# Performance work log

Measured on AMD Instinct MI355X. Metric: run time of the kernel, lower is better.

## Reference

```python
import jax, jax.numpy as jnp
import numpy as np

N = 50000       # nodes
E = 1_600_000   # edges (avg degree 32)
IN = 256        # in_dim
HID = 64        # hidden_dim
HEADS = 2
CLS = 10
NEG_SLOPE = 0.2  # PyG GATConv default leaky_relu slope


def gat_layer(x, edge_index, W, att_src, att_dst, bias, heads, concat):
    """PyG-style GATConv (eval mode, add_self_loops=True).
    x: [N, F_in]; W: [F_in, heads*C]; att_src/att_dst: [heads, C]; bias: [heads*C] or [C].
    """
    n = x.shape[0]
    loop = jnp.arange(n)
    src = jnp.concatenate([edge_index[0], loop])   # message sources j
    dst = jnp.concatenate([edge_index[1], loop])   # message targets i
    C = W.shape[1] // heads
    h = (x @ W).reshape(n, heads, C)               # [N, H, C]
    a_s = jnp.sum(h * att_src, axis=-1)            # [N, H]
    a_d = jnp.sum(h * att_dst, axis=-1)            # [N, H]
    e = jax.nn.leaky_relu(a_s[src] + a_d[dst], NEG_SLOPE)   # [E', H]
    # segment softmax over incoming edges of each destination node
    m = jax.lax.stop_gradient(jax.ops.segment_max(e, dst, num_segments=n))
    ex = jnp.exp(e - m[dst])
    denom = jax.ops.segment_sum(ex, dst, num_segments=n)
    alpha = ex / denom[dst]                         # [E', H]
    out = jax.ops.segment_sum(alpha[:, :, None] * h[src], dst, num_segments=n)  # [N, H, C]
    out = out.reshape(n, heads * C) if concat else out.mean(axis=1)
    return out + bias


def setup_inputs() -> dict:
    key = jax.random.key(0)
    ks = jax.random.split(key, 12)
    sd = lambda f: np.float32(1.0 / np.sqrt(f))
    x = jax.random.normal(ks[0], (N, IN), dtype=jnp.float32)
    edge_index = jax.random.randint(ks[1], (2, E), 0, N, dtype=jnp.int64)
    # layer 1: in_dim -> hidden, heads=2, concat
    W1 = jax.random.normal(ks[2], (IN, HEADS * HID), dtype=jnp.float32) * sd(IN)
    as1 = jax.random.normal(ks[3], (HEADS, HID), dtype=jnp.float32) * sd(HID)
    ad1 = jax.random.normal(ks[4], (HEADS, HID), dtype=jnp.float32) * sd(HID)
    b1 = jnp.zeros((HEADS * HID,), dtype=jnp.float32)
    # layer 2: hidden*heads -> hidden, heads=1, concat=False
    W2 = jax.random.normal(ks[5], (HEADS * HID, HID), dtype=jnp.float32) * sd(HEADS * HID)
    as2 = jax.random.normal(ks[6], (1, HID), dtype=jnp.float32) * sd(HID)
    ad2 = jax.random.normal(ks[7], (1, HID), dtype=jnp.float32) * sd(HID)
    b2 = jnp.zeros((HID,), dtype=jnp.float32)
    # linear head
    Wl = jax.random.normal(ks[8], (HID, CLS), dtype=jnp.float32) * sd(HID)
    bl = jnp.zeros((CLS,), dtype=jnp.float32)
    return {"x": x, "edge_index": edge_index,
            "W1": W1, "as1": as1, "ad1": ad1, "b1": b1,
            "W2": W2, "as2": as2, "ad2": ad2, "b2": b2,
            "Wl": Wl, "bl": bl}


def reference(x, edge_index, W1, as1, ad1, b1, W2, as2, ad2, b2, Wl, bl):
    h = jax.nn.elu(gat_layer(x, edge_index, W1, as1, ad1, b1, HEADS, True))
    h = jax.nn.elu(gat_layer(h, edge_index, W2, as2, ad2, b2, 1, False))
    return h @ Wl + bl  # [N, num_classes]
```

## Files before the change

### kernel.cpp

```cpp
#include <hip/hip_runtime.h>

#define NN 50000
#define NE 1600000
#define EP (NE + NN)
#define IN_DIM 256
#define HIDD 64
#define NCLS 10
#define NBKT 196
#define EPB 8192
#define NPB ((EP + EPB - 1) / EPB)
#define BCAP 12288

typedef unsigned short u16;
typedef short bf16x8 __attribute__((ext_vector_type(8)));
typedef float f32x4 __attribute__((ext_vector_type(4)));

__device__ __forceinline__ float b2f(u16 v) { return __uint_as_float(((unsigned)v) << 16); }
__device__ __forceinline__ u16 f2b(float f) {
    unsigned u = __float_as_uint(f);
    unsigned r = (u + 0x7FFFu + ((u >> 16) & 1u)) >> 16;
    return (u16)r;
}

__device__ __forceinline__ void load_edge(const int* __restrict__ ei, int m, int g,
                                          int& s, int& d) {
    if (g < NE) {
        if (m) { s = ei[2 * (size_t)g]; d = ei[2 * ((size_t)NE + g)]; }
        else   { s = ei[g];             d = ei[NE + g]; }
    } else {
        s = d = g - NE;
    }
    s = s < 0 ? 0 : (s >= NN ? NN - 1 : s);
    d = d < 0 ? 0 : (d >= NN ? NN - 1 : d);
}

__device__ __forceinline__ void wcvt_att_job(
    const float* __restrict__ W, const float* __restrict__ as,
    const float* __restrict__ ad, int K, int N, int H, u16* __restrict__ Wt,
    int idx) {
    if (idx >= K * (N + 16)) return;
    int n = idx / K, k = idx - n * K;
    if (n < N) { Wt[idx] = f2b(W[(size_t)k * N + n]); return; }
    int j = n - N;
    if (j >= 2 * H) { Wt[idx] = 0; return; }
    const float* att = (j & 1) ? ad : as;
    int h = j >> 1, C = N / H;
    float sum = 0.f;
    for (int c = 0; c < C; ++c)
        sum += W[(size_t)k * N + h * C + c] * att[h * C + c];
    Wt[idx] = f2b(sum);
}

__global__ __launch_bounds__(1024) void partition_k(
    const int* __restrict__ ei, int* __restrict__ gcursor,
    unsigned* __restrict__ bbuf,
    const float* __restrict__ W1, const float* __restrict__ as1,
    const float* __restrict__ ad1, u16* __restrict__ w1t,
    const float* __restrict__ W2, const float* __restrict__ as2,
    const float* __restrict__ ad2, u16* __restrict__ w2t,
    const float* __restrict__ Wl, u16* __restrict__ wlt) {
    __shared__ int hist[NBKT], base[NBKT], lbase[NBKT], lcur[NBKT];
    __shared__ int psc[256];
    __shared__ unsigned sst[EPB];
    __shared__ int smode;
    int t = threadIdx.x, b = blockIdx.x;
    if (b < 36) wcvt_att_job(W1, as1, ad1, 256, 128, 2, w1t, b * 1024 + t);
    else if (b < 46) wcvt_att_job(W2, as2, ad2, 128, 64, 1, w2t, (b - 36) * 1024 + t);
    else if (b == 46) {
        int n = t >> 6, k = t & 63;
        wlt[n * 64 + k] = (n < NCLS) ? f2b(Wl[k * NCLS + n]) : (u16)0;
    }
    if (t < 64) {
        int nz = 0;
#pragma unroll
        for (int k = 0; k < 4; ++k)
            if (ei[2 * (t * 4 + k) + 1] != 0) nz = 1;
        unsigned long long bal = __ballot(nz);
        if (t == 0) smode = (bal == 0ULL) ? 1 : 0;
    }
    for (int i = t; i < NBKT; i += 1024) hist[i] = 0;
    __syncthreads();
    int m = smode;
    int g0 = b * EPB;
    int gend = min(g0 + EPB, EP);
    for (int g = g0 + t; g < gend; g += 1024) {
        int s, d;
        load_edge(ei, m, g, s, d);
        atomicAdd(&hist[d >> 8], 1);
    }
    __syncthreads();
    int hv = 0;
    if (t < 256) { hv = (t < NBKT) ? hist[t] : 0; psc[t] = hv; }
    __syncthreads();
    for (int off = 1; off < 256; off <<= 1) {
        int x = (t < 256 && t >= off) ? psc[t - off] : 0;
        __syncthreads();
        if (t < 256) psc[t] += x;
        __syncthreads();
    }
    if (t < NBKT) {
        lbase[t] = psc[t] - hv;
        lcur[t] = 0;
        base[t] = hv ? atomicAdd(&gcursor[t], hv) : 0;
    }
    __syncthreads();
    for (int g = g0 + t; g < gend; g += 1024) {
        int s, d;
        load_edge(ei, m, g, s, d);
        unsigned p = ((unsigned)s << 16) | (unsigned)d;
        int bb = d >> 8;
        int r = lbase[bb] + atomicAdd(&lcur[bb], 1);
        sst[r] = p;
    }
    __syncthreads();
    int cnt = gend - g0;
    for (int l = t; l < cnt; l += 1024) {
        unsigned p = sst[l];
        int bb = (p & 0xFFFF) >> 8;
        int gp = base[bb] + (l - lbase[bb]);
        if (gp < BCAP)
            bbuf[(size_t)bb * BCAP + gp] = ((p >> 16) << 8) | (p & 255u);
    }
}

__global__ __launch_bounds__(1024) void bucket_csr_k(const unsigned* __restrict__ bbuf,
                                                     const int* __restrict__ gcursor,
                                                     int* __restrict__ row_ptr,
                                                     u16* __restrict__ csr_src) {
    __shared__ int bsc[256];
    __shared__ int hist[256], scn[256], cur[256];
    __shared__ int se0, scnt, stot;
    __shared__ u16 srt[BCAP];
    int b = blockIdx.x, t = threadIdx.x;
    int v = 0;
    if (t < 256) {
        v = (t < NBKT) ? min(gcursor[t], BCAP) : 0;
        bsc[t] = v;
        hist[t] = 0;
    }
    __syncthreads();
    for (int off = 1; off < 256; off <<= 1) {
        int x = (t < 256 && t >= off) ? bsc[t - off] : 0;
        __syncthreads();
        if (t < 256) bsc[t] += x;
        __syncthreads();
    }
    if (t == b) { se0 = bsc[t] - v; scnt = v; }
    if (t == NBKT - 1) stot = bsc[t];
    __syncthreads();
    int e0 = se0, cnt = scnt;
    const unsigned* bb = bbuf + (size_t)b * BCAP;
    for (int e = t; e < cnt; e += 1024)
        atomicAdd(&hist[bb[e] & 255], 1);
    __syncthreads();
    int hv = 0;
    if (t < 256) { hv = hist[t]; scn[t] = hv; }
    __syncthreads();
    for (int off = 1; off < 256; off <<= 1) {
        int x = (t < 256 && t >= off) ? scn[t - off] : 0;
        __syncthreads();
        if (t < 256) scn[t] += x;
        __syncthreads();
    }
    if (t < 256) {
        int ex = scn[t] - hv;
        int n = b * 256 + t;
        if (n < NN) row_ptr[n] = e0 + ex;
        cur[t] = ex;
    }
    __syncthreads();
    for (int e = t; e < cnt; e += 1024) {
        unsigned p = bb[e];
        int pos = atomicAdd(&cur[p & 255], 1);
        srt[pos] = (u16)(p >> 8);
    }
    __syncthreads();
    for (int e = t; e < cnt; e += 1024)
        csr_src[e0 + e] = srt[e];
    if (b == 0 && t == 0) row_ptr[NN] = stot;
}

template <int K, int NF, int H, bool F32A, bool SLICED_A, bool SLICED_C>
__global__ __launch_bounds__(256) void gemm_mfma_att_k(
    const float* __restrict__ Af, const u16* __restrict__ Ab,
    const u16* __restrict__ Wt, u16* __restrict__ C,
    float* __restrict__ a_s, float* __restrict__ a_d) {
    constexpr int NTF = NF / 16, NT = NTF + 1, KS = K / 32;
    const int wave = threadIdx.x >> 6, lane = threadIdx.x & 63;
    const int quad = lane >> 4, l15 = lane & 15;
    const int m0 = blockIdx.x * 64 + wave * 16;
    int rowA = m0 + l15;
    if (rowA >= NN) rowA = NN - 1;
    const float* afp = F32A ? (Af + (size_t)rowA * K + quad * 8) : nullptr;
    const u16* abp = nullptr;
    if constexpr (!F32A) {
        abp = SLICED_A ? (Ab + (size_t)rowA * 32 + quad * 8)
                       : (Ab + (size_t)rowA * K + quad * 8);
    }
    const u16* bptr = Wt + (size_t)l15 * K + quad * 8;
    f32x4 acc[NT] = {};
#pragma unroll
    for (int ks = 0; ks < KS; ++ks) {
        bf16x8 af;
        if constexpr (F32A) {
            float4 v0 = *(const float4*)(afp + ks * 32);
            float4 v1 = *(const float4*)(afp + ks * 32 + 4);
            af[0] = (short)f2b(v0.x); af[1] = (short)f2b(v0.y);
            af[2] = (short)f2b(v0.z); af[3] = (short)f2b(v0.w);
            af[4] = (short)f2b(v1.x); af[5] = (short)f2b(v1.y);
            af[6] = (short)f2b(v1.z); af[7] = (short)f2b(v1.w);
        } else {
            af = SLICED_A ? *(const bf16x8*)(abp + (size_t)ks * (NN * 32))
                          : *(const bf16x8*)(abp + ks * 32);
        }
        bf16x8 bf[NT];
#pragma unroll
        for (int nt = 0; nt < NT; ++nt)
            bf[nt] = *(const bf16x8*)(bptr + (size_t)nt * 16 * K + ks * 32);
#pragma unroll
        for (int nt = 0; nt < NT; ++nt)
            acc[nt] = __builtin_amdgcn_mfma_f32_16x16x32_bf16(af, bf[nt], acc[nt], 0, 0, 0);
    }
#pragma unroll
    for (int nt = 0; nt < NTF; ++nt) {
#pragma unroll
        for (int reg = 0; reg < 4; ++reg) {
            int row = m0 + quad * 4 + reg;
            int c = nt * 16 + l15;
            if (row < NN) {
                if constexpr (SLICED_C)
                    C[(size_t)(c >> 5) * (NN * 32) + (size_t)row * 32 + (c & 31)] =
                        f2b(acc[nt][reg]);
                else
                    C[(size_t)row * NF + c] = f2b(acc[nt][reg]);
            }
        }
    }
    if (l15 < 2 * H) {
        int h = l15 >> 1;
        float* dst = (l15 & 1) ? a_d : a_s;
#pragma unroll
        for (int reg = 0; reg < 4; ++reg) {
            int row = m0 + quad * 4 + reg;
            if (row < NN) dst[row * H + h] = acc[NTF][reg];
        }
    }
}

template <int CH, int H, bool HEAD>
__global__ __launch_bounds__(256) void gat_gather_k(
    const int* __restrict__ row_ptr, const u16* __restrict__ csr_src,
    const float* __restrict__ a_s, const float* __restrict__ a_d,
    const u16* __restrict__ h, const float* __restrict__ bias,
    u16* __restrict__ outg, const float* __restrict__ Wl,
    const float* __restrict__ bl, float* __restrict__ outh) {
    constexpr int VEC = CH / 64;
    constexpr int JB = 16;
    int n = (blockIdx.x * blockDim.x + threadIdx.x) >> 6;
    int lane = threadIdx.x & 63;
    if (n >= NN) return;
    int r0 = row_ptr[n], r1 = row_ptr[n + 1];
    const bool hi = (VEC == 2) ? (lane >= 32) : false;
    const int shl16 = hi ? 0 : 16;

    float adn0, adn1 = 0.f;
    if (H == 2) {
        float2 adv = *(const float2*)(a_d + n * 2);
        adn0 = adv.x; adn1 = adv.y;
    } else {
        adn0 = a_d[n];
    }

    float dh0 = 0.f, dh1 = 0.f;
    float acc[VEC];
#pragma unroll
    for (int v = 0; v < VEC; ++v) acc[v] = 0.f;

    for (int base = r0; base < r1; base += 64) {
        int cnt = min(64, r1 - base);
        int idx = base + lane;
        bool act = idx < r1;
        int sl = act ? (int)csr_src[idx] : 0;
        unsigned pex;
        if (H == 2) {
            float2 av = *(const float2*)(a_s + sl * 2);
            float e0 = av.x + adn0;
            e0 = e0 > 0.f ? e0 : 0.2f * e0;
            e0 = fminf(e0, 60.f);
            float ex0 = act ? __expf(e0) : 0.f;
            dh0 += ex0;
            float e1 = av.y + adn1;
            e1 = e1 > 0.f ? e1 : 0.2f * e1;
            e1 = fminf(e1, 60.f);
            float ex1 = act ? __expf(e1) : 0.f;
            dh1 += ex1;
            pex = (unsigned)f2b(ex0) | ((unsigned)f2b(ex1) << 16);
        } else {
            float e0 = a_s[sl] + adn0;
            e0 = e0 > 0.f ? e0 : 0.2f * e0;
            e0 = fminf(e0, 60.f);
            float ex0 = act ? __expf(e0) : 0.f;
            dh0 += ex0;
            pex = (unsigned)sl | ((unsigned)f2b(ex0) << 16);
        }
        for (int j0 = 0; j0 < cnt; j0 += JB) {
            if (VEC == 2) {
                int ssu[JB];
                unsigned peu[JB];
#pragma unroll
                for (int i = 0; i < JB; ++i) {
                    ssu[i] = __builtin_amdgcn_readlane(sl, j0 + i);
                    peu[i] = (unsigned)__builtin_amdgcn_readlane((int)pex, j0 + i);
                }
                unsigned hv[JB];
#pragma unroll
                for (int i = 0; i < JB; ++i)
                    hv[i] = ((const unsigned*)(h + (size_t)ssu[i] * CH))[lane];
#pragma unroll
                for (int i = 0; i < JB; ++i) {
                    float exv = __uint_as_float((peu[i] << shl16) & 0xFFFF0000u);
                    acc[0] += exv * __uint_as_float(hv[i] << 16);
                    acc[1] += exv * __uint_as_float(hv[i] & 0xFFFF0000u);
                }
            } else {
                unsigned peu[JB];
#pragma unroll
                for (int i = 0; i < JB; ++i)
                    peu[i] = (unsigned)__builtin_amdgcn_readlane((int)pex, j0 + i);
                u16 hv[JB];
#pragma unroll
                for (int i = 0; i < JB; ++i)
                    hv[i] = (h + (size_t)(peu[i] & 0xFFFFu) * CH)[lane];
#pragma unroll
                for (int i = 0; i < JB; ++i)
                    acc[0] += __uint_as_float(peu[i] & 0xFFFF0000u) * b2f(hv[i]);
            }
        }
    }

#pragma unroll
    for (int off = 32; off; off >>= 1) dh0 += __shfl_xor(dh0, off);
    float dn = dh0;
    if (H == 2) {
#pragma unroll
        for (int off = 32; off; off >>= 1) dh1 += __shfl_xor(dh1, off);
        dn = hi ? dh1 : dh0;
    }

    if (VEC == 2) {
        int c = lane * 2;
        float2 bv = *(const float2*)(bias + c);
        float v0 = acc[0] / dn + bv.x;
        float v1 = acc[1] / dn + bv.y;
        v0 = v0 > 0.f ? v0 : expm1f(v0);
        v1 = v1 > 0.f ? v1 : expm1f(v1);
        ushort2 ov;
        ov.x = f2b(v0); ov.y = f2b(v1);
        *(ushort2*)(outg + (size_t)(c >> 5) * (NN * 32) + (size_t)n * 32 + (c & 31)) = ov;
    } else {
        float v0 = acc[0] / dn + bias[lane];
        v0 = v0 > 0.f ? v0 : expm1f(v0);
        if (HEAD) {
#pragma unroll
            for (int cls = 0; cls < NCLS; ++cls) {
                float p = v0 * Wl[lane * NCLS + cls];
#pragma unroll
                for (int off = 32; off; off >>= 1) p += __shfl_xor(p, off);
                if (lane == cls) outh[(size_t)n * NCLS + cls] = p + bl[cls];
            }
        } else {
            outg[(size_t)n * CH + lane] = f2b(v0);
        }
    }
}

__global__ __launch_bounds__(256) void edge_alpha_k(
    const int* __restrict__ row_ptr, const u16* __restrict__ csr_src,
    const float* __restrict__ a_s, const float* __restrict__ a_d,
    unsigned* __restrict__ A2, float* __restrict__ dninv) {
    int wave = threadIdx.x >> 6;
    int pair = blockIdx.x * 4 + wave;
    if (pair >= NN / 2) return;
    int lane = threadIdx.x & 63, half = lane >> 5, hl = lane & 31;
    int node = pair * 2 + half;
    int r0 = row_ptr[node], r1 = row_ptr[node + 1];
    int cnt = r1 - r0;
    int co = max(cnt, __shfl_xor(cnt, 32));
    int nbat = (co + 31) >> 5;
    float adn = a_d[node];
    float dh = 0.f;
    for (int b = 0; b < nbat; ++b) {
        int idx = r0 + b * 32 + hl;
        bool act = idx < r1;
        int sl = act ? (int)csr_src[idx] : 0;
        float e = a_s[sl] + adn;
        e = e > 0.f ? e : 0.2f * e;
        e = fminf(e, 60.f);
        float ex = act ? __expf(e) : 0.f;
        dh += ex;
        if (act)
            __builtin_nontemporal_store(
                (unsigned)sl | ((unsigned)f2b(ex) << 16), A2 + idx);
    }
#pragma unroll
    for (int off = 1; off < 32; off <<= 1) dh += __shfl_xor(dh, off);
    if (hl == 0) dninv[node] = 1.0f / dh;
}

template <int CH, int NSL, int H, bool USE_EX>
__global__ __launch_bounds__(256) void gat_slice_k(
    const int* __restrict__ row_ptr, const u16* __restrict__ csr_src,
    const unsigned* __restrict__ A2, const float* __restrict__ a_s,
    const float* __restrict__ a_d, const float* __restrict__ dninv,
    const u16* __restrict__ h, const float* __restrict__ bias,
    u16* __restrict__ outg) {
    constexpr int SC = CH / NSL;
    constexpr int SUB = 8 / NSL;
    int xcd = blockIdx.x & 7;
    int slice = xcd / SUB;
    int sub = xcd % SUB;
    int pg = (blockIdx.x >> 3) * SUB + sub;
    int wave = threadIdx.x >> 6;
    int pair = pg * 4 + wave;
    if (pair >= NN / 2) return;
    int lane = threadIdx.x & 63;
    int half = lane >> 5, hl = lane & 31, q = hl & 7, gh = hl >> 3;
    int node = pair * 2 + half;
    int r0 = row_ptr[node], r1 = row_ptr[node + 1];
    int cnt = r1 - r0;
    int co = max(cnt, __shfl_xor(cnt, 32));
    int nbat = (co + 31) >> 5;
    const unsigned char* hb8 =
        (const unsigned char*)h + (size_t)slice * (NN * 64);
    const int head = (H == 2) ? (slice >> 1) : 0;
    float adn = 0.f, rdn = 0.f;
    if constexpr (USE_EX) rdn = dninv[node];
    else adn = a_d[node * H + head];
    float dh = 0.f;
    float acc[4] = {0.f, 0.f, 0.f, 0.f};
    const int abase = ((half << 5) | gh) << 2;
    for (int b = 0; b < nbat; ++b) {
        int idx = r0 + b * 32 + hl;
        bool act = idx < r1;
        unsigned pex;
        if constexpr (USE_EX) {
            pex = act ? __builtin_nontemporal_load(A2 + idx) : 0u;
        } else {
            int sl = act ? (int)__builtin_nontemporal_load(csr_src + idx) : 0;
            float e = a_s[sl * H + head] + adn;
            e = e > 0.f ? e : 0.2f * e;
            e = fminf(e, 60.f);
            float ex = act ? __expf(e) : 0.f;
            dh += ex;
            pex = (unsigned)sl | ((unsigned)f2b(ex) << 16);
        }
#pragma unroll
        for (int jr = 0; jr < 2; ++jr) {
            int pr[4];
#pragma unroll
            for (int i = 0; i < 4; ++i)
                pr[i] = __builtin_amdgcn_ds_bpermute(
                    abase + ((jr * 16 + i * 4) << 2), (int)pex);
            unsigned hv0[4], hv1[4];
#pragma unroll
            for (int i = 0; i < 4; ++i) {
                const unsigned* p = (const unsigned*)(
                    hb8 + (((unsigned)((unsigned)pr[i] & 0xFFFFu) << 6) + q * 8));
                hv0[i] = p[0];
                hv1[i] = p[1];
            }
#pragma unroll
            for (int i = 0; i < 4; ++i) {
                float exf = __uint_as_float((unsigned)pr[i] & 0xFFFF0000u);
                unsigned w0 = hv0[i], w1 = hv1[i];
                acc[0] += exf * __uint_as_float(w0 << 16);
                acc[1] += exf * __uint_as_float(w0 & 0xFFFF0000u);
                acc[2] += exf * __uint_as_float(w1 << 16);
                acc[3] += exf * __uint_as_float(w1 & 0xFFFF0000u);
            }
        }
    }
    if constexpr (!USE_EX) {
#pragma unroll
        for (int off = 1; off < 32; off <<= 1) dh += __shfl_xor(dh, off);
        rdn = 1.0f / dh;
    }
#pragma unroll
    for (int v = 0; v < 4; ++v) {
        acc[v] += __shfl_xor(acc[v], 8);
        acc[v] += __shfl_xor(acc[v], 16);
    }
    if (gh == 0) {
        float vv[4];
#pragma unroll
        for (int k = 0; k < 4; ++k) {
            float t = acc[k] * rdn + bias[slice * SC + q * 4 + k];
            vv[k] = t > 0.f ? t : expm1f(t);
        }
        unsigned long long ov =
            (unsigned long long)((unsigned)f2b(vv[0]) | ((unsigned)f2b(vv[1]) << 16)) |
            ((unsigned long long)((unsigned)f2b(vv[2]) | ((unsigned)f2b(vv[3]) << 16)) << 32);
        __builtin_nontemporal_store(
            ov, (unsigned long long*)(outg + (size_t)slice * (NN * 32) +
                                      (size_t)node * 32 + q * 4));
    }
}

__global__ __launch_bounds__(256) void head_gemm_k(
    const u16* __restrict__ A, const u16* __restrict__ Wt,
    const float* __restrict__ bl, float* __restrict__ out) {
    const int wave = threadIdx.x >> 6, lane = threadIdx.x & 63;
    const int quad = lane >> 4, l15 = lane & 15;
    const int m0 = blockIdx.x * 64 + wave * 16;
    int rowA = m0 + l15;
    if (rowA >= NN) rowA = NN - 1;
    const u16* ab = A + (size_t)rowA * 32 + quad * 8;
    const u16* bp = Wt + (size_t)l15 * 64 + quad * 8;
    f32x4 acc = {};
#pragma unroll
    for (int ks = 0; ks < 2; ++ks) {
        bf16x8 af = *(const bf16x8*)(ab + (size_t)ks * (NN * 32));
        bf16x8 bf = *(const bf16x8*)(bp + ks * 32);
        acc = __builtin_amdgcn_mfma_f32_16x16x32_bf16(af, bf, acc, 0, 0, 0);
    }
    if (l15 < NCLS) {
        float blv = bl[l15];
#pragma unroll
        for (int reg = 0; reg < 4; ++reg) {
            int row = m0 + quad * 4 + reg;
            if (row < NN) out[(size_t)row * NCLS + l15] = acc[reg] + blv;
        }
    }
}

extern "C" void kernel_launch(void* const* d_in, const int* in_sizes, int n_in,
                              void* d_out, int out_size, void* d_ws, size_t ws_size,
                              hipStream_t stream) {
    const float* x   = (const float*)d_in[0];
    const int*   ei  = (const int*)d_in[1];
    const float* W1  = (const float*)d_in[2];
    const float* as1 = (const float*)d_in[3];
    const float* ad1 = (const float*)d_in[4];
    const float* b1  = (const float*)d_in[5];
    const float* W2  = (const float*)d_in[6];
    const float* as2 = (const float*)d_in[7];
    const float* ad2 = (const float*)d_in[8];
    const float* b2  = (const float*)d_in[9];
    const float* Wl  = (const float*)d_in[10];
    const float* bl  = (const float*)d_in[11];
    float* out = (float*)d_out;

    float* ws = (float*)d_ws;
    size_t o = 0;
    u16* hb  = (u16*)(ws + o); o += (size_t)NN * 64;
    u16* g2  = hb + (size_t)NN * 64;
    u16* g1  = (u16*)(ws + o); o += (size_t)NN * 64;
    unsigned* bbuf = (unsigned*)g1;
    unsigned* A2 = (unsigned*)g1;
    float* dn2inv = (float*)((char*)g1 + (size_t)EP * 4);
    u16* w1t = (u16*)(ws + o); o += 144 * 256 / 2;
    u16* w2t = (u16*)(ws + o); o += 80 * 128 / 2;
    u16* wlt = (u16*)(ws + o); o += 16 * 64 / 2;
    float* a_s = ws + o;       o += (size_t)NN * 2;
    float* a_d = ws + o;       o += (size_t)NN * 2;
    int* ints = (int*)(ws + o);
    size_t io = 0;
    int* gcursor  = ints + io; io += NBKT;
    int* row_ptr  = ints + io; io += NN + 1;
    u16* csr_src  = (u16*)(ints + io); io += (EP + 1) / 2;

    hipMemsetAsync(gcursor, 0, NBKT * sizeof(int), stream);
    partition_k<<<NPB, 1024, 0, stream>>>(ei, gcursor, bbuf,
                                          W1, as1, ad1, w1t, W2, as2, ad2, w2t,
                                          Wl, wlt);
    bucket_csr_k<<<NBKT, 1024, 0, stream>>>(bbuf, gcursor, row_ptr, csr_src);

    const int gemmBlocks = (NN + 63) / 64;
    const int gatherBlocks = (NN + 3) / 4;

    gemm_mfma_att_k<256, 128, 2, true, false, false><<<gemmBlocks, 256, 0, stream>>>(
        x, nullptr, w1t, hb, a_s, a_d);
    gat_gather_k<128, 2, false><<<gatherBlocks, 256, 0, stream>>>(
        row_ptr, csr_src, a_s, a_d, hb, b1, g1, nullptr, nullptr, nullptr);

    gemm_mfma_att_k<128, 64, 1, false, true, true><<<gemmBlocks, 256, 0, stream>>>(
        nullptr, g1, w2t, hb, a_s, a_d);
    edge_alpha_k<<<(NN / 2 + 3) / 4, 256, 0, stream>>>(
        row_ptr, csr_src, a_s, a_d, A2, dn2inv);
    gat_slice_k<64, 2, 1, true><<<12504, 256, 0, stream>>>(
        row_ptr, csr_src, A2, nullptr, nullptr, dn2inv, hb, b2, g2);

    head_gemm_k<<<gemmBlocks, 256, 0, stream>>>(g2, wlt, bl, out);
}
```

Measured before the change: 304.2 us.

## Merge edge partition with first GEMM in one launch and cache edges in registers

```diff
diff --git a/kernel.cpp b/kernel.cpp
--- a/kernel.cpp
+++ b/kernel.cpp
@@ -7,7 +7,7 @@
 #define HIDD 64
 #define NCLS 10
 #define NBKT 196
-#define EPB 8192
+#define EPB 2048
 #define NPB ((EP + EPB - 1) / EPB)
 #define BCAP 12288
 
@@ -51,25 +51,33 @@
     Wt[idx] = f2b(sum);
 }
 
-__global__ __launch_bounds__(1024) void partition_k(
-    const int* __restrict__ ei, int* __restrict__ gcursor,
-    unsigned* __restrict__ bbuf,
+__global__ __launch_bounds__(256) void wcvt_k(
     const float* __restrict__ W1, const float* __restrict__ as1,
     const float* __restrict__ ad1, u16* __restrict__ w1t,
     const float* __restrict__ W2, const float* __restrict__ as2,
     const float* __restrict__ ad2, u16* __restrict__ w2t,
-    const float* __restrict__ Wl, u16* __restrict__ wlt) {
+    const float* __restrict__ Wl, u16* __restrict__ wlt,
+    int* __restrict__ gcursor) {
+    int b = blockIdx.x, t = threadIdx.x;
+    if (b < 144) wcvt_att_job(W1, as1, ad1, 256, 128, 2, w1t, b * 256 + t);
+    else if (b < 184) wcvt_att_job(W2, as2, ad2, 128, 64, 1, w2t, (b - 144) * 256 + t);
+    else if (b < 188) {
+        int idx = (b - 184) * 256 + t;
+        int n = idx >> 6, k = idx & 63;
+        wlt[n * 64 + k] = (n < NCLS) ? f2b(Wl[k * NCLS + n]) : (u16)0;
+    } else {
+        if (t < NBKT) gcursor[t] = 0;
+    }
+}
+
+__device__ void partition_body(int b, const int* __restrict__ ei,
+                               int* __restrict__ gcursor,
+                               unsigned* __restrict__ bbuf) {
     __shared__ int hist[NBKT], base[NBKT], lbase[NBKT], lcur[NBKT];
     __shared__ int psc[256];
     __shared__ unsigned sst[EPB];
     __shared__ int smode;
-    int t = threadIdx.x, b = blockIdx.x;
-    if (b < 36) wcvt_att_job(W1, as1, ad1, 256, 128, 2, w1t, b * 1024 + t);
-    else if (b < 46) wcvt_att_job(W2, as2, ad2, 128, 64, 1, w2t, (b - 36) * 1024 + t);
-    else if (b == 46) {
-        int n = t >> 6, k = t & 63;
-        wlt[n * 64 + k] = (n < NCLS) ? f2b(Wl[k * NCLS + n]) : (u16)0;
-    }
+    int t = threadIdx.x;
     if (t < 64) {
         int nz = 0;
 #pragma unroll
@@ -78,24 +86,49 @@
         unsigned long long bal = __ballot(nz);
         if (t == 0) smode = (bal == 0ULL) ? 1 : 0;
     }
-    for (int i = t; i < NBKT; i += 1024) hist[i] = 0;
+    for (int i = t; i < NBKT; i += 256) hist[i] = 0;
     __syncthreads();
     int m = smode;
-    int g0 = b * EPB;
-    int gend = min(g0 + EPB, EP);
-    for (int g = g0 + t; g < gend; g += 1024) {
-        int s, d;
-        load_edge(ei, m, g, s, d);
-        atomicAdd(&hist[d >> 8], 1);
-    }
-    __syncthreads();
-    int hv = 0;
-    if (t < 256) { hv = (t < NBKT) ? hist[t] : 0; psc[t] = hv; }
+    int g0 = b * EPB, gend = min(g0 + EPB, EP);
+    unsigned ed[8];
+#pragma unroll
+    for (int i = 0; i < 4; ++i) {
+        int g = g0 + i * 512 + 2 * t;
+        int s0 = 0, d0 = 0, s1 = 0, d1 = 0;
+        bool v0 = g < gend, v1 = g + 1 < gend;
+        if (v1 && g >= NE) {
+            s0 = d0 = g - NE; s1 = d1 = g + 1 - NE;
+        } else if (v1 && g + 1 < NE) {
+            if (m) {
+                int4 sv = *(const int4*)(ei + 2 * (size_t)g);
+                int4 dv = *(const int4*)(ei + 2 * ((size_t)NE + g));
+                s0 = sv.x; s1 = sv.z; d0 = dv.x; d1 = dv.z;
+            } else {
+                int2 sv = *(const int2*)(ei + g);
+                int2 dv = *(const int2*)(ei + NE + g);
+                s0 = sv.x; s1 = sv.y; d0 = dv.x; d1 = dv.y;
+            }
+            s0 = s0 < 0 ? 0 : (s0 >= NN ? NN - 1 : s0);
+            d0 = d0 < 0 ? 0 : (d0 >= NN ? NN - 1 : d0);
+            s1 = s1 < 0 ? 0 : (s1 >= NN ? NN - 1 : s1);
+            d1 = d1 < 0 ? 0 : (d1 >= NN ? NN - 1 : d1);
+        } else {
+            if (v0) load_edge(ei, m, g, s0, d0);
+            if (v1) load_edge(ei, m, g + 1, s1, d1);
+        }
+        if (v0) { ed[2 * i] = ((unsigned)s0 << 16) | (unsigned)d0; atomicAdd(&hist[d0 >> 8], 1); }
+        else ed[2 * i] = 0xFFFFFFFFu;
+        if (v1) { ed[2 * i + 1] = ((unsigned)s1 << 16) | (unsigned)d1; atomicAdd(&hist[d1 >> 8], 1); }
+        else ed[2 * i + 1] = 0xFFFFFFFFu;
+    }
+    __syncthreads();
+    int hv = (t < NBKT) ? hist[t] : 0;
+    psc[t] = hv;
     __syncthreads();
     for (int off = 1; off < 256; off <<= 1) {
-        int x = (t < 256 && t >= off) ? psc[t - off] : 0;
+        int x = (t >= off) ? psc[t - off] : 0;
         __syncthreads();
-        if (t < 256) psc[t] += x;
+        psc[t] += x;
         __syncthreads();
     }
     if (t < NBKT) {
@@ -104,23 +137,109 @@
         base[t] = hv ? atomicAdd(&gcursor[t], hv) : 0;
     }
     __syncthreads();
-    for (int g = g0 + t; g < gend; g += 1024) {
-        int s, d;
-        load_edge(ei, m, g, s, d);
-        unsigned p = ((unsigned)s << 16) | (unsigned)d;
-        int bb = d >> 8;
-        int r = lbase[bb] + atomicAdd(&lcur[bb], 1);
-        sst[r] = p;
+#pragma unroll
+    for (int i = 0; i < 8; ++i) {
+        unsigned p = ed[i];
+        if (p != 0xFFFFFFFFu) {
+            int bb = (p & 0xFFFF) >> 8;
+            int r = lbase[bb] + atomicAdd(&lcur[bb], 1);
+            sst[r] = p;
+        }
     }
     __syncthreads();
     int cnt = gend - g0;
-    for (int l = t; l < cnt; l += 1024) {
+    for (int l = t; l < cnt; l += 256) {
         unsigned p = sst[l];
         int bb = (p & 0xFFFF) >> 8;
         int gp = base[bb] + (l - lbase[bb]);
         if (gp < BCAP)
             bbuf[(size_t)bb * BCAP + gp] = ((p >> 16) << 8) | (p & 255u);
     }
+}
+
+template <int K, int NF, int H, bool F32A, bool SLICED_A, bool SLICED_C>
+__device__ __forceinline__ void gemm_body(
+    int bb, const float* __restrict__ Af, const u16* __restrict__ Ab,
+    const u16* __restrict__ Wt, u16* __restrict__ C,
+    float* __restrict__ a_s, float* __restrict__ a_d) {
+    constexpr int NTF = NF / 16, NT = NTF + 1, KS = K / 32;
+    const int wave = threadIdx.x >> 6, lane = threadIdx.x & 63;
+    const int quad = lane >> 4, l15 = lane & 15;
+    const int m0 = bb * 64 + wave * 16;
+    int rowA = m0 + l15;
+    if (rowA >= NN) rowA = NN - 1;
+    const float* afp = F32A ? (Af + (size_t)rowA * K + quad * 8) : nullptr;
+    const u16* abp = nullptr;
+    if constexpr (!F32A) {
+        abp = SLICED_A ? (Ab + (size_t)rowA * 32 + quad * 8)
+                       : (Ab + (size_t)rowA * K + quad * 8);
+    }
+    const u16* bptr = Wt + (size_t)l15 * K + quad * 8;
+    f32x4 acc[NT] = {};
+#pragma unroll
+    for (int ks = 0; ks < KS; ++ks) {
+        bf16x8 af;
+        if constexpr (F32A) {
+            float4 v0 = *(const float4*)(afp + ks * 32);
+            float4 v1 = *(const float4*)(afp + ks * 32 + 4);
+            af[0] = (short)f2b(v0.x); af[1] = (short)f2b(v0.y);
+            af[2] = (short)f2b(v0.z); af[3] = (short)f2b(v0.w);
+            af[4] = (short)f2b(v1.x); af[5] = (short)f2b(v1.y);
+            af[6] = (short)f2b(v1.z); af[7] = (short)f2b(v1.w);
+        } else {
+            af = SLICED_A ? *(const bf16x8*)(abp + (size_t)ks * (NN * 32))
+                          : *(const bf16x8*)(abp + ks * 32);
+        }
+        bf16x8 bf[NT];
+#pragma unroll
+        for (int nt = 0; nt < NT; ++nt)
+            bf[nt] = *(const bf16x8*)(bptr + (size_t)nt * 16 * K + ks * 32);
+#pragma unroll
+        for (int nt = 0; nt < NT; ++nt)
+            acc[nt] = __builtin_amdgcn_mfma_f32_16x16x32_bf16(af, bf[nt], acc[nt], 0, 0, 0);
+    }
+#pragma unroll
+    for (int nt = 0; nt < NTF; ++nt) {
+#pragma unroll
+        for (int reg = 0; reg < 4; ++reg) {
+            int row = m0 + quad * 4 + reg;
+            int c = nt * 16 + l15;
+            if (row < NN) {
+                if constexpr (SLICED_C)
+                    C[(size_t)(c >> 5) * (NN * 32) + (size_t)row * 32 + (c & 31)] =
+                        f2b(acc[nt][reg]);
+                else
+                    C[(size_t)row * NF + c] = f2b(acc[nt][reg]);
+            }
+        }
+    }
+    if (l15 < 2 * H) {
+        int h = l15 >> 1;
+        float* dst = (l15 & 1) ? a_d : a_s;
+#pragma unroll
+        for (int reg = 0; reg < 4; ++reg) {
+            int row = m0 + quad * 4 + reg;
+            if (row < NN) dst[row * H + h] = acc[NTF][reg];
+        }
+    }
+}
+
+__global__ __launch_bounds__(256) void part_gemm_k(
+    const int* __restrict__ ei, int* __restrict__ gcursor,
+    unsigned* __restrict__ bbuf, const float* __restrict__ x,
+    const u16* __restrict__ w1t, u16* __restrict__ hb,
+    float* __restrict__ a_s, float* __restrict__ a_d) {
+    if (blockIdx.x < NPB)
+        partition_body(blockIdx.x, ei, gcursor, bbuf);
+    else
+        gemm_body<256, 128, 2, true, false, false>(blockIdx.x - NPB, x, nullptr,
+                                                   w1t, hb, a_s, a_d);
+}
+
+__global__ __launch_bounds__(256) void gemm2_k(
+    const u16* __restrict__ Ab, const u16* __restrict__ Wt, u16* __restrict__ C,
+    float* __restrict__ a_s, float* __restrict__ a_d) {
+    gemm_body<128, 64, 1, false, true, true>(blockIdx.x, nullptr, Ab, Wt, C, a_s, a_d);
 }
 
 __global__ __launch_bounds__(1024) void bucket_csr_k(const unsigned* __restrict__ bbuf,
@@ -178,73 +297,6 @@
     for (int e = t; e < cnt; e += 1024)
         csr_src[e0 + e] = srt[e];
     if (b == 0 && t == 0) row_ptr[NN] = stot;
-}
-
-template <int K, int NF, int H, bool F32A, bool SLICED_A, bool SLICED_C>
-__global__ __launch_bounds__(256) void gemm_mfma_att_k(
-    const float* __restrict__ Af, const u16* __restrict__ Ab,
-    const u16* __restrict__ Wt, u16* __restrict__ C,
-    float* __restrict__ a_s, float* __restrict__ a_d) {
-    constexpr int NTF = NF / 16, NT = NTF + 1, KS = K / 32;
-    const int wave = threadIdx.x >> 6, lane = threadIdx.x & 63;
-    const int quad = lane >> 4, l15 = lane & 15;
-    const int m0 = blockIdx.x * 64 + wave * 16;
-    int rowA = m0 + l15;
-    if (rowA >= NN) rowA = NN - 1;
-    const float* afp = F32A ? (Af + (size_t)rowA * K + quad * 8) : nullptr;
-    const u16* abp = nullptr;
-    if constexpr (!F32A) {
-        abp = SLICED_A ? (Ab + (size_t)rowA * 32 + quad * 8)
-                       : (Ab + (size_t)rowA * K + quad * 8);
-    }
-    const u16* bptr = Wt + (size_t)l15 * K + quad * 8;
-    f32x4 acc[NT] = {};
-#pragma unroll
-    for (int ks = 0; ks < KS; ++ks) {
-        bf16x8 af;
-        if constexpr (F32A) {
-            float4 v0 = *(const float4*)(afp + ks * 32);
-            float4 v1 = *(const float4*)(afp + ks * 32 + 4);
-            af[0] = (short)f2b(v0.x); af[1] = (short)f2b(v0.y);
-            af[2] = (short)f2b(v0.z); af[3] = (short)f2b(v0.w);
-            af[4] = (short)f2b(v1.x); af[5] = (short)f2b(v1.y);
-            af[6] = (short)f2b(v1.z); af[7] = (short)f2b(v1.w);
-        } else {
-            af = SLICED_A ? *(const bf16x8*)(abp + (size_t)ks * (NN * 32))
-                          : *(const bf16x8*)(abp + ks * 32);
-        }
-        bf16x8 bf[NT];
-#pragma unroll
-        for (int nt = 0; nt < NT; ++nt)
-            bf[nt] = *(const bf16x8*)(bptr + (size_t)nt * 16 * K + ks * 32);
-#pragma unroll
-        for (int nt = 0; nt < NT; ++nt)
-            acc[nt] = __builtin_amdgcn_mfma_f32_16x16x32_bf16(af, bf[nt], acc[nt], 0, 0, 0);
-    }
-#pragma unroll
-    for (int nt = 0; nt < NTF; ++nt) {
-#pragma unroll
-        for (int reg = 0; reg < 4; ++reg) {
-            int row = m0 + quad * 4 + reg;
-            int c = nt * 16 + l15;
-            if (row < NN) {
-                if constexpr (SLICED_C)
-                    C[(size_t)(c >> 5) * (NN * 32) + (size_t)row * 32 + (c & 31)] =
-                        f2b(acc[nt][reg]);
-                else
-                    C[(size_t)row * NF + c] = f2b(acc[nt][reg]);
-            }
-        }
-    }
-    if (l15 < 2 * H) {
-        int h = l15 >> 1;
-        float* dst = (l15 & 1) ? a_d : a_s;
-#pragma unroll
-        for (int reg = 0; reg < 4; ++reg) {
-            int row = m0 + quad * 4 + reg;
-            if (row < NN) dst[row * H + h] = acc[NTF][reg];
-        }
-    }
 }
 
 template <int CH, int H, bool HEAD>
@@ -569,26 +621,20 @@
     int* row_ptr  = ints + io; io += NN + 1;
     u16* csr_src  = (u16*)(ints + io); io += (EP + 1) / 2;
 
-    hipMemsetAsync(gcursor, 0, NBKT * sizeof(int), stream);
-    partition_k<<<NPB, 1024, 0, stream>>>(ei, gcursor, bbuf,
-                                          W1, as1, ad1, w1t, W2, as2, ad2, w2t,
-                                          Wl, wlt);
-    bucket_csr_k<<<NBKT, 1024, 0, stream>>>(bbuf, gcursor, row_ptr, csr_src);
-
     const int gemmBlocks = (NN + 63) / 64;
     const int gatherBlocks = (NN + 3) / 4;
 
-    gemm_mfma_att_k<256, 128, 2, true, false, false><<<gemmBlocks, 256, 0, stream>>>(
-        x, nullptr, w1t, hb, a_s, a_d);
+    wcvt_k<<<189, 256, 0, stream>>>(W1, as1, ad1, w1t, W2, as2, ad2, w2t,
+                                    Wl, wlt, gcursor);
+    part_gemm_k<<<NPB + gemmBlocks, 256, 0, stream>>>(
+        ei, gcursor, bbuf, x, w1t, hb, a_s, a_d);
+    bucket_csr_k<<<NBKT, 1024, 0, stream>>>(bbuf, gcursor, row_ptr, csr_src);
     gat_gather_k<128, 2, false><<<gatherBlocks, 256, 0, stream>>>(
         row_ptr, csr_src, a_s, a_d, hb, b1, g1, nullptr, nullptr, nullptr);
-
-    gemm_mfma_att_k<128, 64, 1, false, true, true><<<gemmBlocks, 256, 0, stream>>>(
-        nullptr, g1, w2t, hb, a_s, a_d);
+    gemm2_k<<<gemmBlocks, 256, 0, stream>>>(g1, w2t, hb, a_s, a_d);
     edge_alpha_k<<<(NN / 2 + 3) / 4, 256, 0, stream>>>(
         row_ptr, csr_src, a_s, a_d, A2, dn2inv);
     gat_slice_k<64, 2, 1, true><<<12504, 256, 0, stream>>>(
         row_ptr, csr_src, A2, nullptr, nullptr, dn2inv, hb, b2, g2);
-
     head_gemm_k<<<gemmBlocks, 256, 0, stream>>>(g2, wlt, bl, out);
 }
```

New measurement: 305.8 us. Within noise of the previous version (+0.5%).

## Drop edge-alpha precompute kernel and cache bucket entries in registers during CSR sort

Applied to the files above, without the earlier changes.

```diff
diff --git a/kernel.cpp b/kernel.cpp
--- a/kernel.cpp
+++ b/kernel.cpp
@@ -150,8 +150,18 @@
     __syncthreads();
     int e0 = se0, cnt = scnt;
     const unsigned* bb = bbuf + (size_t)b * BCAP;
-    for (int e = t; e < cnt; e += 1024)
-        atomicAdd(&hist[bb[e] & 255], 1);
+    unsigned ed[BCAP / 1024];
+#pragma unroll
+    for (int i = 0; i < BCAP / 1024; ++i) {
+        int e = t + i * 1024;
+        if (e < cnt) {
+            unsigned p = bb[e];
+            ed[i] = p;
+            atomicAdd(&hist[p & 255], 1);
+        } else {
+            ed[i] = 0xFFFFFFFFu;
+        }
+    }
     __syncthreads();
     int hv = 0;
     if (t < 256) { hv = hist[t]; scn[t] = hv; }
@@ -169,10 +179,13 @@
         cur[t] = ex;
     }
     __syncthreads();
-    for (int e = t; e < cnt; e += 1024) {
-        unsigned p = bb[e];
-        int pos = atomicAdd(&cur[p & 255], 1);
-        srt[pos] = (u16)(p >> 8);
+#pragma unroll
+    for (int i = 0; i < BCAP / 1024; ++i) {
+        unsigned p = ed[i];
+        if (p != 0xFFFFFFFFu) {
+            int pos = atomicAdd(&cur[p & 255], 1);
+            srt[pos] = (u16)(p >> 8);
+        }
     }
     __syncthreads();
     for (int e = t; e < cnt; e += 1024)
@@ -372,39 +385,6 @@
             outg[(size_t)n * CH + lane] = f2b(v0);
         }
     }
-}
-
-__global__ __launch_bounds__(256) void edge_alpha_k(
-    const int* __restrict__ row_ptr, const u16* __restrict__ csr_src,
-    const float* __restrict__ a_s, const float* __restrict__ a_d,
-    unsigned* __restrict__ A2, float* __restrict__ dninv) {
-    int wave = threadIdx.x >> 6;
-    int pair = blockIdx.x * 4 + wave;
-    if (pair >= NN / 2) return;
-    int lane = threadIdx.x & 63, half = lane >> 5, hl = lane & 31;
-    int node = pair * 2 + half;
-    int r0 = row_ptr[node], r1 = row_ptr[node + 1];
-    int cnt = r1 - r0;
-    int co = max(cnt, __shfl_xor(cnt, 32));
-    int nbat = (co + 31) >> 5;
-    float adn = a_d[node];
-    float dh = 0.f;
-    for (int b = 0; b < nbat; ++b) {
-        int idx = r0 + b * 32 + hl;
-        bool act = idx < r1;
-        int sl = act ? (int)csr_src[idx] : 0;
-        float e = a_s[sl] + adn;
-        e = e > 0.f ? e : 0.2f * e;
-        e = fminf(e, 60.f);
-        float ex = act ? __expf(e) : 0.f;
-        dh += ex;
-        if (act)
-            __builtin_nontemporal_store(
-                (unsigned)sl | ((unsigned)f2b(ex) << 16), A2 + idx);
-    }
-#pragma unroll
-    for (int off = 1; off < 32; off <<= 1) dh += __shfl_xor(dh, off);
-    if (hl == 0) dninv[node] = 1.0f / dh;
 }
 
 template <int CH, int NSL, int H, bool USE_EX>
@@ -556,8 +536,6 @@
     u16* g2  = hb + (size_t)NN * 64;
     u16* g1  = (u16*)(ws + o); o += (size_t)NN * 64;
     unsigned* bbuf = (unsigned*)g1;
-    unsigned* A2 = (unsigned*)g1;
-    float* dn2inv = (float*)((char*)g1 + (size_t)EP * 4);
     u16* w1t = (u16*)(ws + o); o += 144 * 256 / 2;
     u16* w2t = (u16*)(ws + o); o += 80 * 128 / 2;
     u16* wlt = (u16*)(ws + o); o += 16 * 64 / 2;
@@ -585,10 +563,8 @@
 
     gemm_mfma_att_k<128, 64, 1, false, true, true><<<gemmBlocks, 256, 0, stream>>>(
         nullptr, g1, w2t, hb, a_s, a_d);
-    edge_alpha_k<<<(NN / 2 + 3) / 4, 256, 0, stream>>>(
-        row_ptr, csr_src, a_s, a_d, A2, dn2inv);
-    gat_slice_k<64, 2, 1, true><<<12504, 256, 0, stream>>>(
-        row_ptr, csr_src, A2, nullptr, nullptr, dn2inv, hb, b2, g2);
+    gat_slice_k<64, 2, 1, false><<<12504, 256, 0, stream>>>(
+        row_ptr, csr_src, nullptr, a_s, a_d, nullptr, hb, b2, g2);
 
     head_gemm_k<<<gemmBlocks, 256, 0, stream>>>(g2, wlt, bl, out);
 }
```

Result: no change. 300.1 us (-1.4%).
